# Kernel tuning notes

Hardware: AMD Instinct MI355X
Metric: run time of the kernel (lower is better)

The kernel has to match this reference:

```python
import jax, jax.numpy as jnp
import numpy as np

TAU = 0.02        # System2Reasoner softmax temperature
TOP_K = 50        # retrieval top-k
ALPHA = 1.0       # visual/text prototype mixing
TAU_CONF = 0.8    # entropy confidence threshold


def _normalize(x):
    return x / jnp.maximum(jnp.linalg.norm(x, axis=-1, keepdims=True), 1e-12)


def _entropy(logits):
    p = jax.nn.softmax(logits, axis=-1)
    return -jnp.sum(p * jnp.log(p + 1e-10))


def setup_inputs() -> dict:
    key = jax.random.key(0)
    k1, k2, k3, k4, k5, k6 = jax.random.split(key, 6)
    D, P, M, C = 768, 2048, 65536, 1000
    test_global = _normalize(jax.random.normal(k1, (1, D), dtype=jnp.float32))
    test_patches = _normalize(jax.random.normal(k2, (P, D), dtype=jnp.float32))
    memory_nodes = _normalize(jax.random.normal(k3, (M, D), dtype=jnp.float32))
    textual_anchors = _normalize(jax.random.normal(k4, (C, D), dtype=jnp.float32))
    class_sums = jax.random.normal(k5, (C, D), dtype=jnp.float32)
    class_counts = jax.random.uniform(k6, (C,), dtype=jnp.float32) * 100.0 + 1.0
    return {
        "test_global": test_global,
        "test_patches": test_patches,
        "memory_nodes": memory_nodes,
        "textual_anchors": textual_anchors,
        "class_sums": class_sums,
        "class_counts": class_counts,
        "max_steps": 3,
    }


def reference(test_global, test_patches, memory_nodes, textual_anchors,
              class_sums, class_counts, max_steps):
    # System-1 prototypes
    safe_counts = jnp.maximum(class_counts, 1.0)[:, None]            # [C,1]
    visual_protos = _normalize(class_sums / safe_counts)             # [C,D]
    protos = _normalize(textual_anchors + ALPHA * visual_protos)     # [C,D]

    sys1_logits = 100.0 * test_global @ protos.T                     # [1,C]
    active0 = _entropy(sys1_logits) > TAU_CONF

    def body(carry, _):
        patches, logits, step, active = carry
        # message passing: topk cosine-sim retrieval + softmax-weighted gather
        sim = patches @ memory_nodes.T                               # [P,M]
        topv, topi = jax.lax.top_k(sim, TOP_K)                       # [P,K]
        attn = jax.nn.softmax(topv / TAU, axis=1)                    # [P,K]
        gathered = memory_nodes[topi]                                # [P,K,D]
        messages = jnp.einsum('pk,pkd->pd', attn, gathered)          # [P,D]
        new_patches = _normalize(patches + messages)
        # token evidence pooling
        ev = jnp.max(new_patches @ textual_anchors.T, axis=-1, keepdims=True)  # [P,1]
        w = jax.nn.softmax(ev / TAU, axis=0)                         # [P,1]
        g = _normalize(jnp.sum(new_patches * w, axis=0, keepdims=True))        # [1,D]
        new_logits = 100.0 * g @ protos.T                            # [1,C]
        # only commit updates while the entropy loop is still active
        patches = jnp.where(active, new_patches, patches)
        logits = jnp.where(active, new_logits, logits)
        step = step + active.astype(jnp.int32)
        active = jnp.logical_and(active, _entropy(new_logits) > TAU_CONF)
        return (patches, logits, step, active), None

    (patches, final_logits, step, _), _ = jax.lax.scan(
        body, (test_patches, sys1_logits, jnp.int32(0), active0),
        None, length=max_steps)
    return final_logits, step
```

## Files before the change

### kernel.cpp

```cpp
#include <hip/hip_runtime.h>
#include <hip/hip_bf16.h>
#include <stdint.h>


typedef __attribute__((ext_vector_type(8))) short short8;
typedef __attribute__((ext_vector_type(4))) float f32x4;

#define DIM    768
#define NPATCH 2048
#define NMEM   65536
#define NCLS   1000
#define NSAMP  4096
#define CAP    1024
#define PRESEL 64
#define PCAP   128
#define TAUINV 50.0f

__device__ __forceinline__ unsigned short f2bf(float f){
  unsigned b = __float_as_uint(f);
  b += 0x7FFFu + ((b >> 16) & 1u);
  return (unsigned short)(b >> 16);
}
__device__ __forceinline__ unsigned encf(float x){
  unsigned b = __float_as_uint(x);
  return (b & 0x80000000u) ? ~b : (b | 0x80000000u);
}
__device__ __forceinline__ float decf(unsigned k){
  unsigned b = (k & 0x80000000u) ? (k & 0x7FFFFFFFu) : ~k;
  return __uint_as_float(b);
}
__device__ __forceinline__ void gload16(const void* g, void* l){
  __builtin_amdgcn_global_load_lds(
      (const __attribute__((address_space(1))) unsigned int*)g,
      (__attribute__((address_space(3))) unsigned int*)l, 16, 0, 0);
}
__device__ __forceinline__ uint4 pack8(float4 a, float4 b){
  uint4 u;
  u.x = (unsigned)f2bf(a.x) | ((unsigned)f2bf(a.y) << 16);
  u.y = (unsigned)f2bf(a.z) | ((unsigned)f2bf(a.w) << 16);
  u.z = (unsigned)f2bf(b.x) | ((unsigned)f2bf(b.y) << 16);
  u.w = (unsigned)f2bf(b.z) | ((unsigned)f2bf(b.w) << 16);
  return u;
}

__device__ __forceinline__ unsigned select_kth(const unsigned* keys, int n, int k,
                                               unsigned* hist, int t)
{
  __syncthreads();
  if (t == 0){ hist[256] = 0u; hist[257] = (unsigned)k; }
  __syncthreads();
  for (int pass = 0; pass < 4; ++pass){
    int shift = 24 - 8*pass;
    hist[t] = 0u;
    __syncthreads();
    unsigned pref = hist[256];
    for (int i = t; i < n; i += 256){
      unsigned key = keys[i];
      bool ok = (pass == 0) || ((key >> (shift + 8)) == pref);
      if (ok) atomicAdd(&hist[(key >> shift) & 255u], 1u);
    }
    __syncthreads();
    if (t == 0){
      unsigned krem = hist[257];
      unsigned cum = 0u; int b = 255;
      for (; b >= 0; --b){ cum += hist[b]; if (cum >= krem) break; }
      if (b < 0) b = 0;
      unsigned above = cum - hist[b];
      hist[257] = krem - above;
      hist[256] = (pref << 8) | (unsigned)b;
    }
    __syncthreads();
  }
  return hist[256];
}

__global__ __launch_bounds__(256) void proto_kernel(
    const float* __restrict__ anchors, const float* __restrict__ sums,
    const float* __restrict__ counts, float* __restrict__ protos,
    unsigned short* __restrict__ anchors_bf)
{
  int c = blockIdx.x, t = threadIdx.x;
  if (c >= NCLS){
    for (int j = 0; j < 3; ++j) anchors_bf[(size_t)c*DIM + t + j*256] = 0;
    return;
  }
  __shared__ float wv[4]; __shared__ float bc;
  float cnt = fmaxf(counts[c], 1.0f);
  float v[3];
  #pragma unroll
  for (int j = 0; j < 3; ++j) v[j] = sums[(size_t)c*DIM + t + j*256] / cnt;
  float ss = v[0]*v[0] + v[1]*v[1] + v[2]*v[2];
  for (int off = 32; off > 0; off >>= 1) ss += __shfl_down(ss, off, 64);
  if ((t & 63) == 0) wv[t >> 6] = ss;
  __syncthreads();
  if (t == 0) bc = wv[0] + wv[1] + wv[2] + wv[3];
  __syncthreads();
  float rn = 1.0f / fmaxf(sqrtf(bc), 1e-12f);
  __syncthreads();
  float pr[3];
  #pragma unroll
  for (int j = 0; j < 3; ++j){
    int d = t + j*256;
    float a = anchors[(size_t)c*DIM + d];
    pr[j] = a + v[j] * rn;
    int dd = (d & ~63) | ((((d >> 3) ^ c) & 7) << 3) | (d & 7);
    anchors_bf[(size_t)c*DIM + dd] = f2bf(a);
  }
  ss = pr[0]*pr[0] + pr[1]*pr[1] + pr[2]*pr[2];
  for (int off = 32; off > 0; off >>= 1) ss += __shfl_down(ss, off, 64);
  if ((t & 63) == 0) wv[t >> 6] = ss;
  __syncthreads();
  if (t == 0) bc = wv[0] + wv[1] + wv[2] + wv[3];
  __syncthreads();
  float rn2 = 1.0f / fmaxf(sqrtf(bc), 1e-12f);
  #pragma unroll
  for (int j = 0; j < 3; ++j) protos[(size_t)c*DIM + t + j*256] = pr[j] * rn2;
}

__global__ __launch_bounds__(256) void prep_patches(
    const float* __restrict__ tp, float* __restrict__ pc)
{
  size_t i = (size_t)blockIdx.x*256 + threadIdx.x;
  *(float4*)(pc + i*4) = *(const float4*)(tp + i*4);
}

__global__ __launch_bounds__(256) void conv_kernel(
    const float* __restrict__ src, unsigned short* __restrict__ dst)
{
  int id = blockIdx.x*256 + threadIdx.x;
  int row = id / 12, blk = id % 12;
  const float4* s = (const float4*)(src + (size_t)row*DIM + blk*64);
  unsigned short* drow = dst + (size_t)row*DIM + blk*64;
  int key = row & 7;
  #pragma unroll
  for (int c8 = 0; c8 < 8; ++c8){
    uint4 u = pack8(s[c8*2], s[c8*2+1]);
    *(uint4*)(drow + (c8 ^ key)*8) = u;
  }
}

__global__ __launch_bounds__(192) void slab_kernel(
    const float* __restrict__ pc, unsigned short* __restrict__ slab)
{
  int b = blockIdx.x, t = threadIdx.x;
  int p = b*2 + (t >= 96 ? 1 : 0);
  int q = (t >= 96) ? t - 96 : t;
  int ks = q >> 3, c8 = q & 7;
  const float* s = pc + (size_t)p*DIM + ks*64 + c8*8;
  uint4 u = pack8(*(const float4*)s, *(const float4*)(s + 4));
  *(uint4*)((char*)slab + (((size_t)ks*NPATCH + p)*128) + ((size_t)(c8 ^ (p & 7))*16)) = u;
}

template<int MODE, int NT>
__global__ __launch_bounds__(256, 3) void gemm_kernel(
    const unsigned short* __restrict__ Abf, int rowbase,
    const unsigned short* __restrict__ Bslab,
    const float* __restrict__ thresholds,
    int* __restrict__ counters,
    int* __restrict__ cand_idx,
    float* __restrict__ cand_score,
    float* __restrict__ sims_sample,
    unsigned* __restrict__ ev_key,
    const int* __restrict__ active)
{
  if (*active == 0) return;
  __shared__ __align__(16) unsigned short Al[128*64];
  __shared__ __align__(16) unsigned short Bl[128*64];
  int b = blockIdx.x, nwg = gridDim.x;
  int wg = (b & 7)*(nwg >> 3) + (b >> 3);
  int mt0 = (wg >> 4) * NT, pt = wg & 15;
  int t = threadIdx.x, w = t >> 6, lane = t & 63, l15 = lane & 15, l4 = lane >> 4;
  int wr = w >> 1, wc = w & 1;
  int pbase = pt*128;
  int srow = w*8 + (lane >> 3);
  int scol = (lane & 7)*16;

  const char* Ab = (const char*)Abf;
  const char* Bb = (const char*)Bslab;

  float thv[4];
  if (MODE == 0){
    #pragma unroll
    for (int g = 0; g < 4; ++g) thv[g] = thresholds[pbase + wc*64 + g*16 + l15];
  }

  f32x4 acc[4][4];
  #pragma unroll
  for (int x = 0; x < 4; ++x)
    #pragma unroll
    for (int y = 0; y < 4; ++y) acc[x][y] = (f32x4){0.f, 0.f, 0.f, 0.f};

  const int NSTEP = NT * 12;
  for (int s = 0; s < NSTEP; ++s){
    int tile = s / 12, ks = s % 12;
    if (s) __syncthreads();
    size_t arow0 = (size_t)rowbase + ((size_t)(mt0 + tile))*128;
    #pragma unroll
    for (int i = 0; i < 4; ++i){
      const void* ga = Ab + ((arow0 + srow + i*32)*(size_t)(DIM*2)) + ks*128 + scol;
      gload16(ga, (char*)Al + i*4096 + w*1024);
      const void* gb = Bb + (((size_t)ks*NPATCH + pbase)*128) + i*4096 + w*1024 + lane*16;
      gload16(gb, (char*)Bl + i*4096 + w*1024);
    }
    __syncthreads();

    short8 af[2][4], bf_[2][4];
    #pragma unroll
    for (int kk = 0; kk < 2; ++kk){
      #pragma unroll
      for (int ng = 0; ng < 4; ++ng){
        int row = wr*64 + ng*16 + l15;
        int slot = (kk*4 + l4) ^ (row & 7);
        af[kk][ng] = *(const short8*)((const char*)Al + row*128 + slot*16);
      }
      #pragma unroll
      for (int g = 0; g < 4; ++g){
        int row = wc*64 + g*16 + l15;
        int slot = (kk*4 + l4) ^ (row & 7);
        bf_[kk][g] = *(const short8*)((const char*)Bl + row*128 + slot*16);
      }
    }
    #pragma unroll
    for (int kk = 0; kk < 2; ++kk)
      #pragma unroll
      for (int ng = 0; ng < 4; ++ng)
        #pragma unroll
        for (int g = 0; g < 4; ++g)
          acc[ng][g] = __builtin_amdgcn_mfma_f32_16x16x32_bf16(af[kk][ng], bf_[kk][g], acc[ng][g], 0, 0, 0);

    if (ks == 11){
      int nodebase = rowbase + (mt0 + tile)*128 + wr*64;
      if (MODE == 0){
        #pragma unroll
        for (int g = 0; g < 4; ++g){
          int patch = pbase + wc*64 + g*16 + l15;
          float th = thv[g];
          #pragma unroll
          for (int ng = 0; ng < 4; ++ng){
            #pragma unroll
            for (int i = 0; i < 4; ++i){
              float v = acc[ng][g][i];
              if (v >= th){
                int node = nodebase + ng*16 + l4*4 + i;
                int pos = atomicAdd(&counters[patch], 1);
                if (pos < CAP){
                  cand_idx[(size_t)patch*CAP + pos]   = node;
                  cand_score[(size_t)patch*CAP + pos] = v;
                }
              }
            }
          }
        }
      } else if (MODE == 1){
        #pragma unroll
        for (int g = 0; g < 4; ++g){
          int patch = pbase + wc*64 + g*16 + l15;
          #pragma unroll
          for (int ng = 0; ng < 4; ++ng){
            int col = nodebase + ng*16 + l4*4;
            *(f32x4*)(sims_sample + (size_t)patch*NSAMP + col) = acc[ng][g];
          }
        }
      } else {
        #pragma unroll
        for (int g = 0; g < 4; ++g){
          int patch = pbase + wc*64 + g*16 + l15;
          float m = -3e38f; bool any = false;
          #pragma unroll
          for (int ng = 0; ng < 4; ++ng){
            #pragma unroll
            for (int i = 0; i < 4; ++i){
              int a = nodebase + ng*16 + l4*4 + i;
              if (a < NCLS){ m = fmaxf(m, acc[ng][g][i]); any = true; }
            }
          }
          if (any) atomicMax(&ev_key[patch], encf(m));
        }
      }
      if (tile + 1 < NT){
        #pragma unroll
        for (int x = 0; x < 4; ++x)
          #pragma unroll
          for (int y = 0; y < 4; ++y) acc[x][y] = (f32x4){0.f, 0.f, 0.f, 0.f};
      }
    }
  }
}

__global__ __launch_bounds__(256) void thresh_kernel(
    const float* __restrict__ sims, float* __restrict__ thresholds,
    int* __restrict__ counters, int* __restrict__ cand_idx,
    float* __restrict__ cand_score, unsigned* __restrict__ ev_key,
    const int* __restrict__ active)
{
  if (*active == 0) return;
  __shared__ unsigned keys[NSAMP];
  __shared__ unsigned hist[258];
  __shared__ int lcnt;
  int p = blockIdx.x, t = threadIdx.x;
  const float4* src = (const float4*)(sims + (size_t)p*NSAMP);
  for (int i = t; i < NSAMP/4; i += 256){
    float4 v = src[i];
    keys[i*4+0] = encf(v.x); keys[i*4+1] = encf(v.y);
    keys[i*4+2] = encf(v.z); keys[i*4+3] = encf(v.w);
  }
  unsigned kth = select_kth(keys, NSAMP, 16, hist, t);
  if (t == 0){ thresholds[p] = decf(kth); ev_key[p] = 0u; lcnt = 0; }
  __syncthreads();
  for (int i = t; i < NSAMP; i += 256){
    unsigned key = keys[i];
    if (key >= kth){
      int pos = atomicAdd(&lcnt, 1);
      if (pos < CAP){
        cand_idx[(size_t)p*CAP + pos]   = i;
        cand_score[(size_t)p*CAP + pos] = decf(key);
      }
    }
  }
  __syncthreads();
  if (t == 0) counters[p] = lcnt < CAP ? lcnt : CAP;
}

__global__ __launch_bounds__(256) void msg_kernel(
    const int* __restrict__ counters, const int* __restrict__ cand_idx,
    const float* __restrict__ cand_score, const float* __restrict__ memf,
    float* __restrict__ pc, unsigned short* __restrict__ slab,
    const int* __restrict__ active)
{
  if (*active == 0) return;
  __shared__ unsigned sk[CAP]; __shared__ int si[CAP];
  __shared__ __align__(16) float gl[DIM];
  __shared__ unsigned hist[258];
  __shared__ int pn[PCAP]; __shared__ float pv[PCAP];
  __shared__ float selv[64]; __shared__ int seli[64]; __shared__ float attn[64];
  __shared__ float wv[4]; __shared__ float bc;
  __shared__ int cnt2;
  int p = blockIdx.x, t = threadIdx.x;
  int n = counters[p]; if (n > CAP) n = CAP;
  #pragma unroll
  for (int j = 0; j < 3; ++j) gl[t + j*256] = pc[(size_t)p*DIM + t + j*256];
  for (int i = t; i < CAP; i += 256){
    sk[i] = (i < n) ? encf(cand_score[(size_t)p*CAP + i]) : 0u;
    si[i] = (i < n) ? cand_idx[(size_t)p*CAP + i] : 0;
  }
  unsigned kth64 = 1u;
  if (n > PRESEL) kth64 = select_kth(sk, n, PRESEL, hist, t);
  else            __syncthreads();
  if (t == 0) cnt2 = 0;
  __syncthreads();
  for (int i = t; i < n; i += 256){
    if (sk[i] >= kth64){
      int pos = atomicAdd(&cnt2, 1);
      if (pos < PCAP) pn[pos] = si[i];
    }
  }
  __syncthreads();
  int m = cnt2 < PCAP ? cnt2 : PCAP;
  int w = t >> 6, lane = t & 63;
  for (int i = w; i < m; i += 4){
    const float* row = memf + (size_t)pn[i]*DIM;
    float s = 0.f;
    #pragma unroll
    for (int j = 0; j < 12; ++j){
      int d = lane + j*64;
      s += row[d] * gl[d];
    }
    for (int off = 32; off > 0; off >>= 1) s += __shfl_down(s, off, 64);
    if (lane == 0) pv[i] = s;
  }
  __syncthreads();
  int K = m < 50 ? m : 50;
  if (t < m) sk[t] = encf(pv[t]);
  unsigned kth50 = 1u;
  if (m > K) kth50 = select_kth(sk, m, K, hist, t);
  else       __syncthreads();
  if (t == 0) cnt2 = 0;
  __syncthreads();
  if (t < m && sk[t] > kth50){
    int pos = atomicAdd(&cnt2, 1);
    seli[pos] = pn[t]; selv[pos] = pv[t];
    sk[t] = 0u;
  }
  __syncthreads();
  if (t == 0){
    int c = cnt2;
    for (int j = c; j < K; ++j){
      int best = -1, bestnode = 0x7FFFFFFF;
      for (int i = 0; i < m; ++i)
        if (sk[i] == kth50 && pn[i] < bestnode){ best = i; bestnode = pn[i]; }
      if (best < 0) break;
      seli[j] = pn[best]; selv[j] = pv[best]; sk[best] = 0u;
    }
  }
  __syncthreads();
  float v = (t < K) ? selv[t] : -3e38f;
  for (int off = 32; off > 0; off >>= 1) v = fmaxf(v, __shfl_down(v, off, 64));
  if ((t & 63) == 0) wv[t >> 6] = v;
  __syncthreads();
  if (t == 0) bc = fmaxf(fmaxf(wv[0], wv[1]), fmaxf(wv[2], wv[3]));
  __syncthreads();
  float vmax = bc;
  __syncthreads();
  if (t < K) attn[t] = __expf((selv[t] - vmax) * TAUINV);
  __syncthreads();
  if (t == 0){ float s = 0.f; for (int k = 0; k < K; ++k) s += attn[k]; bc = s; }
  __syncthreads();
  float inv = 1.0f / bc;
  int d0 = t, d1 = t + 256, d2 = t + 512;
  float a0 = gl[d0], a1 = gl[d1], a2 = gl[d2];
  for (int k = 0; k < K; ++k){
    float a = attn[k] * inv;
    const float* row = memf + (size_t)seli[k]*DIM;
    a0 += a * row[d0]; a1 += a * row[d1]; a2 += a * row[d2];
  }
  float ss = a0*a0 + a1*a1 + a2*a2;
  for (int off = 32; off > 0; off >>= 1) ss += __shfl_down(ss, off, 64);
  if ((t & 63) == 0) wv[t >> 6] = ss;
  __syncthreads();
  if (t == 0) bc = wv[0] + wv[1] + wv[2] + wv[3];
  __syncthreads();
  float rn = 1.0f / fmaxf(sqrtf(bc), 1e-12f);
  a0 *= rn; a1 *= rn; a2 *= rn;
  float* orow = pc + (size_t)p*DIM;
  orow[d0] = a0; orow[d1] = a1; orow[d2] = a2;
  __syncthreads();
  gl[d0] = a0; gl[d1] = a1; gl[d2] = a2;
  __syncthreads();
  if (t < 96){
    int ks2 = t >> 3, c8 = t & 7;
    const float* sblk = &gl[ks2*64 + c8*8];
    uint4 u = pack8(*(const float4*)sblk, *(const float4*)(sblk + 4));
    *(uint4*)((char*)slab + (((size_t)ks2*NPATCH + p)*128) + ((size_t)(c8 ^ (p & 7))*16)) = u;
  }
}

__global__ __launch_bounds__(256) void pl2_kernel(
    const unsigned* __restrict__ ev_key, const float* __restrict__ pc,
    float* __restrict__ g_part, const int* __restrict__ active)
{
  if (*active == 0) return;
  __shared__ float wv[4]; __shared__ float bc;
  int t = threadIdx.x;
  float m = -3e38f;
  for (int i = t; i < NPATCH; i += 256) m = fmaxf(m, decf(ev_key[i]));
  for (int off = 32; off > 0; off >>= 1) m = fmaxf(m, __shfl_down(m, off, 64));
  if ((t & 63) == 0) wv[t >> 6] = m;
  __syncthreads();
  if (t == 0) bc = fmaxf(fmaxf(wv[0], wv[1]), fmaxf(wv[2], wv[3]));
  __syncthreads();
  float M = bc;
  __syncthreads();
  float s = 0.f;
  for (int i = t; i < NPATCH; i += 256) s += __expf((decf(ev_key[i]) - M) * TAUINV);
  for (int off = 32; off > 0; off >>= 1) s += __shfl_down(s, off, 64);
  if ((t & 63) == 0) wv[t >> 6] = s;
  __syncthreads();
  if (t == 0) bc = wv[0] + wv[1] + wv[2] + wv[3];
  __syncthreads();
  float invS = 1.0f / bc;
  int pbase = blockIdx.x * 64;
  float a0 = 0.f, a1 = 0.f, a2 = 0.f;
  for (int i = 0; i < 64; ++i){
    int p = pbase + i;
    float wgt = __expf((decf(ev_key[p]) - M) * TAUINV) * invS;
    const float* row = pc + (size_t)p*DIM;
    a0 += wgt * row[t]; a1 += wgt * row[t + 256]; a2 += wgt * row[t + 512];
  }
  g_part[blockIdx.x*DIM + t]       = a0;
  g_part[blockIdx.x*DIM + t + 256] = a1;
  g_part[blockIdx.x*DIM + t + 512] = a2;
}

template<bool INIT>
__global__ __launch_bounds__(256) void cm_kernel(
    const float* __restrict__ gsrc, const float* __restrict__ protos,
    float* __restrict__ logits_cur, int* __restrict__ step, int* __restrict__ active)
{
  if (!INIT && *active == 0) return;
  __shared__ __align__(16) float gl[DIM];
  __shared__ float lg[NCLS];
  __shared__ float wv[4]; __shared__ float bc;
  int t = threadIdx.x;
  if (INIT){
    #pragma unroll
    for (int j = 0; j < 3; ++j) gl[t + j*256] = gsrc[t + j*256];
  } else {
    float gv[3]; float ss = 0.f;
    #pragma unroll
    for (int j = 0; j < 3; ++j){
      int d = t + j*256;
      float s = 0.f;
      for (int b2 = 0; b2 < 32; ++b2) s += gsrc[b2*DIM + d];
      gv[j] = s; ss += s*s;
    }
    for (int off = 32; off > 0; off >>= 1) ss += __shfl_down(ss, off, 64);
    if ((t & 63) == 0) wv[t >> 6] = ss;
    __syncthreads();
    if (t == 0) bc = wv[0] + wv[1] + wv[2] + wv[3];
    __syncthreads();
    float rn = 1.0f / fmaxf(sqrtf(bc), 1e-12f);
    #pragma unroll
    for (int j = 0; j < 3; ++j) gl[t + j*256] = gv[j] * rn;
  }
  __syncthreads();
  for (int c = t; c < NCLS; c += 256){
    const float4* pr = (const float4*)(protos + (size_t)c*DIM);
    float s = 0.f;
    #pragma unroll 4
    for (int d4 = 0; d4 < DIM/4; ++d4){
      float4 pv = pr[d4];
      float4 gv = *(const float4*)&gl[d4*4];
      s += gv.x*pv.x + gv.y*pv.y + gv.z*pv.z + gv.w*pv.w;
    }
    float L = 100.0f * s;
    lg[c] = L; logits_cur[c] = L;
  }
  __syncthreads();
  float m = -3e38f;
  for (int c = t; c < NCLS; c += 256) m = fmaxf(m, lg[c]);
  for (int off = 32; off > 0; off >>= 1) m = fmaxf(m, __shfl_down(m, off, 64));
  if ((t & 63) == 0) wv[t >> 6] = m;
  __syncthreads();
  if (t == 0) bc = fmaxf(fmaxf(wv[0], wv[1]), fmaxf(wv[2], wv[3]));
  __syncthreads();
  float M = bc;
  __syncthreads();
  float s = 0.f;
  for (int c = t; c < NCLS; c += 256) s += __expf(lg[c] - M);
  for (int off = 32; off > 0; off >>= 1) s += __shfl_down(s, off, 64);
  if ((t & 63) == 0) wv[t >> 6] = s;
  __syncthreads();
  if (t == 0) bc = wv[0] + wv[1] + wv[2] + wv[3];
  __syncthreads();
  float S = bc;
  __syncthreads();
  float hp = 0.f;
  for (int c = t; c < NCLS; c += 256){
    float pcl = __expf(lg[c] - M) / S;
    hp += pcl * __logf(pcl + 1e-10f);
  }
  for (int off = 32; off > 0; off >>= 1) hp += __shfl_down(hp, off, 64);
  if ((t & 63) == 0) wv[t >> 6] = hp;
  __syncthreads();
  if (t == 0){
    float H = -(wv[0] + wv[1] + wv[2] + wv[3]);
    if (INIT){ *step = 0; *active = (H > 0.8f) ? 1 : 0; }
    else     { *step = *step + 1; *active = (H > 0.8f) ? 1 : 0; }
  }
}

__global__ void pub_kernel(const float* __restrict__ logits_cur, const int* __restrict__ step,
                           float* __restrict__ out)
{
  int i = blockIdx.x*256 + threadIdx.x;
  if (i < NCLS) out[i] = logits_cur[i];
  else if (i == NCLS) out[i] = (float)(*step);
}

extern "C" void kernel_launch(void* const* d_in, const int* in_sizes, int n_in,
                              void* d_out, int out_size, void* d_ws, size_t ws_size,
                              hipStream_t stream)
{
  (void)in_sizes; (void)n_in; (void)out_size; (void)ws_size;
  const float* tg  = (const float*)d_in[0];
  const float* tp  = (const float*)d_in[1];
  const float* mem = (const float*)d_in[2];
  const float* anc = (const float*)d_in[3];
  const float* cs  = (const float*)d_in[4];
  const float* cc  = (const float*)d_in[5];

  char* ws = (char*)d_ws;
  auto al = [](size_t x){ return (x + 255) & ~(size_t)255; };
  size_t OFF_PC   = 0;
  size_t OFF_PROT = al(OFF_PC   + (size_t)NPATCH*DIM*4);
  size_t OFF_ABF  = al(OFF_PROT + (size_t)NCLS*DIM*4);
  size_t OFF_MBF  = al(OFF_ABF  + (size_t)1024*DIM*2);
  size_t OFF_SLAB = al(OFF_MBF  + (size_t)NMEM*DIM*2);
  size_t OFF_SS   = al(OFF_SLAB + (size_t)NPATCH*DIM*2);
  size_t OFF_THR  = al(OFF_SS   + (size_t)NPATCH*NSAMP*4);
  size_t OFF_CNT  = al(OFF_THR  + (size_t)NPATCH*4);
  size_t OFF_CI   = al(OFF_CNT  + (size_t)NPATCH*4);
  size_t OFF_CSC  = al(OFF_CI   + (size_t)NPATCH*CAP*4);
  size_t OFF_EV   = al(OFF_CSC  + (size_t)NPATCH*CAP*4);
  size_t OFF_GP   = al(OFF_EV   + (size_t)NPATCH*4);
  size_t OFF_LC   = al(OFF_GP   + (size_t)32*DIM*4);
  size_t OFF_STEP = al(OFF_LC   + (size_t)NCLS*4);

  float*          pc      = (float*)(ws + OFF_PC);
  float*          protos  = (float*)(ws + OFF_PROT);
  unsigned short* abf     = (unsigned short*)(ws + OFF_ABF);
  unsigned short* mbf     = (unsigned short*)(ws + OFF_MBF);
  unsigned short* slab    = (unsigned short*)(ws + OFF_SLAB);
  float*          simss   = (float*)(ws + OFF_SS);
  float*          thr     = (float*)(ws + OFF_THR);
  int*            cnt     = (int*)(ws + OFF_CNT);
  int*            ci      = (int*)(ws + OFF_CI);
  float*          csc     = (float*)(ws + OFF_CSC);
  unsigned*       evk     = (unsigned*)(ws + OFF_EV);
  float*          gp      = (float*)(ws + OFF_GP);
  float*          lc      = (float*)(ws + OFF_LC);
  int*            stepp   = (int*)(ws + OFF_STEP);
  int*            activep = stepp + 1;

  proto_kernel<<<1024, 256, 0, stream>>>(anc, cs, cc, protos, abf);
  prep_patches<<<(NPATCH*DIM/4)/256, 256, 0, stream>>>(tp, pc);
  conv_kernel<<<(NMEM*12)/256, 256, 0, stream>>>(mem, mbf);
  cm_kernel<true><<<1, 256, 0, stream>>>(tg, protos, lc, stepp, activep);
  slab_kernel<<<NPATCH/2, 192, 0, stream>>>(pc, slab);

  for (int it = 0; it < 3; ++it){
    gemm_kernel<1,1><<<(NSAMP/128)*16, 256, 0, stream>>>(mbf, 0, slab, thr, cnt, ci, csc, simss, evk, activep);
    thresh_kernel<<<NPATCH, 256, 0, stream>>>(simss, thr, cnt, ci, csc, evk, activep);
    gemm_kernel<0,4><<<((NMEM-NSAMP)/512)*16, 256, 0, stream>>>(mbf, NSAMP, slab, thr, cnt, ci, csc, simss, evk, activep);
    msg_kernel<<<NPATCH, 256, 0, stream>>>(cnt, ci, csc, mem, pc, slab, activep);
    gemm_kernel<2,1><<<(1024/128)*16, 256, 0, stream>>>(abf, 0, slab, thr, cnt, ci, csc, simss, evk, activep);
    pl2_kernel<<<32, 256, 0, stream>>>(evk, pc, gp, activep);
    cm_kernel<false><<<1, 256, 0, stream>>>(gp, protos, lc, stepp, activep);
  }
  pub_kernel<<<4, 256, 0, stream>>>(lc, stepp, (float*)d_out);
}
```

Measured before the change: 2.010 ms.

## Quantize memory nodes and patches to int8 for retrieval similarity GEMMs

Memory nodes and patches are now quantized to int8 with per-row scales, and the sampling and candidate-threshold GEMMs use i8 MFMA (16x16x64) instead of bf16. Scores are rescaled in the epilogue before thresholding and candidate collection. The evidence GEMM against text anchors stays in bf16 as a separate kernel. This halves the operand bytes and doubles MFMA throughput per instruction. The cost is coarser similarity estimates, which may shift thresholds and candidate sets, although the final messages are still computed from fp32 scores.

```diff
diff --git a/kernel.cpp b/kernel.cpp
--- a/kernel.cpp
+++ b/kernel.cpp
@@ -5,6 +5,7 @@
 
 typedef __attribute__((ext_vector_type(8))) short short8;
 typedef __attribute__((ext_vector_type(4))) float f32x4;
+typedef __attribute__((ext_vector_type(4))) int   i32x4;
 
 #define DIM    768
 #define NPATCH 2048
@@ -42,6 +43,21 @@
   u.w = (unsigned)f2bf(b.z) | ((unsigned)f2bf(b.w) << 16);
   return u;
 }
+__device__ __forceinline__ uint4 packq16(const float* s, float inv){
+  unsigned wd[4];
+  #pragma unroll
+  for (int k = 0; k < 4; ++k){
+    unsigned v = 0;
+    #pragma unroll
+    for (int j = 0; j < 4; ++j){
+      int q = __float2int_rn(s[k*4 + j] * inv);
+      q = q > 127 ? 127 : (q < -127 ? -127 : q);
+      v |= ((unsigned)(q & 255)) << (8*j);
+    }
+    wd[k] = v;
+  }
+  return make_uint4(wd[0], wd[1], wd[2], wd[3]);
+}
 
 __device__ __forceinline__ unsigned select_kth(const unsigned* keys, int n, int k,
                                                unsigned* hist, int t)
@@ -124,71 +140,98 @@
   *(float4*)(pc + i*4) = *(const float4*)(tp + i*4);
 }
 
-__global__ __launch_bounds__(256) void conv_kernel(
-    const float* __restrict__ src, unsigned short* __restrict__ dst)
-{
-  int id = blockIdx.x*256 + threadIdx.x;
-  int row = id / 12, blk = id % 12;
-  const float4* s = (const float4*)(src + (size_t)row*DIM + blk*64);
-  unsigned short* drow = dst + (size_t)row*DIM + blk*64;
-  int key = row & 7;
-  #pragma unroll
-  for (int c8 = 0; c8 < 8; ++c8){
-    uint4 u = pack8(s[c8*2], s[c8*2+1]);
-    *(uint4*)(drow + (c8 ^ key)*8) = u;
-  }
-}
-
-__global__ __launch_bounds__(192) void slab_kernel(
-    const float* __restrict__ pc, unsigned short* __restrict__ slab)
-{
-  int b = blockIdx.x, t = threadIdx.x;
-  int p = b*2 + (t >= 96 ? 1 : 0);
-  int q = (t >= 96) ? t - 96 : t;
-  int ks = q >> 3, c8 = q & 7;
-  const float* s = pc + (size_t)p*DIM + ks*64 + c8*8;
-  uint4 u = pack8(*(const float4*)s, *(const float4*)(s + 4));
-  *(uint4*)((char*)slab + (((size_t)ks*NPATCH + p)*128) + ((size_t)(c8 ^ (p & 7))*16)) = u;
+__global__ __launch_bounds__(512) void conv_i8_kernel(
+    const float* __restrict__ src, signed char* __restrict__ dst,
+    float* __restrict__ scales)
+{
+  int w = threadIdx.x >> 6, lane = threadIdx.x & 63;
+  int row = blockIdx.x*8 + w;
+  const float* r = src + (size_t)row*DIM;
+  float x[16]; float mx = 0.f;
+  if (lane < 48){
+    #pragma unroll
+    for (int j = 0; j < 4; ++j){
+      float4 v = *(const float4*)(r + lane*16 + j*4);
+      x[j*4+0] = v.x; x[j*4+1] = v.y; x[j*4+2] = v.z; x[j*4+3] = v.w;
+      mx = fmaxf(mx, fmaxf(fmaxf(fabsf(v.x), fabsf(v.y)), fmaxf(fabsf(v.z), fabsf(v.w))));
+    }
+  }
+  for (int off = 32; off > 0; off >>= 1) mx = fmaxf(mx, __shfl_xor(mx, off, 64));
+  if (lane == 0) scales[row] = mx / 127.0f;
+  float inv = (mx > 0.f) ? 127.0f / mx : 0.f;
+  if (lane < 48){
+    int ks = lane >> 2, c = lane & 3;
+    uint4 u = packq16(x, inv);
+    *(uint4*)(dst + (size_t)row*DIM + ks*64 + ((c ^ (row & 3))*16)) = u;
+  }
+}
+
+__global__ __launch_bounds__(256) void slab_init(
+    const float* __restrict__ pc, unsigned short* __restrict__ slab,
+    signed char* __restrict__ sli8, float* __restrict__ spb)
+{
+  __shared__ __align__(16) float gl[DIM];
+  __shared__ float wv[4]; __shared__ float bc;
+  int p = blockIdx.x, t = threadIdx.x;
+  float a0 = pc[(size_t)p*DIM + t], a1 = pc[(size_t)p*DIM + t + 256],
+        a2 = pc[(size_t)p*DIM + t + 512];
+  gl[t] = a0; gl[t + 256] = a1; gl[t + 512] = a2;
+  float am = fmaxf(fabsf(a0), fmaxf(fabsf(a1), fabsf(a2)));
+  for (int off = 32; off > 0; off >>= 1) am = fmaxf(am, __shfl_down(am, off, 64));
+  if ((t & 63) == 0) wv[t >> 6] = am;
+  __syncthreads();
+  if (t == 0) bc = fmaxf(fmaxf(wv[0], wv[1]), fmaxf(wv[2], wv[3]));
+  __syncthreads();
+  float mx = bc;
+  float inv8 = (mx > 0.f) ? 127.0f / mx : 0.f;
+  if (t < 96){
+    int ks2 = t >> 3, c8 = t & 7;
+    const float* sblk = &gl[ks2*64 + c8*8];
+    uint4 u = pack8(*(const float4*)sblk, *(const float4*)(sblk + 4));
+    *(uint4*)((char*)slab + (((size_t)ks2*NPATCH + p)*128) + ((size_t)(c8 ^ (p & 7))*16)) = u;
+  }
+  if (t < 48){
+    int ks2 = t >> 2, c = t & 3;
+    uint4 u = packq16(&gl[t*16], inv8);
+    *(uint4*)(sli8 + ((size_t)ks2*NPATCH + p)*64 + ((c ^ (p & 3))*16)) = u;
+  }
+  if (t == 0) spb[p] = mx / 127.0f;
 }
 
 template<int MODE, int NT>
-__global__ __launch_bounds__(256, 3) void gemm_kernel(
-    const unsigned short* __restrict__ Abf, int rowbase,
-    const unsigned short* __restrict__ Bslab,
+__global__ __launch_bounds__(256, 3) void gemm8_kernel(
+    const signed char* __restrict__ Ai8, const float* __restrict__ sA, int rowbase,
+    const signed char* __restrict__ Bslab, const float* __restrict__ sB,
     const float* __restrict__ thresholds,
     int* __restrict__ counters,
     int* __restrict__ cand_idx,
     float* __restrict__ cand_score,
     float* __restrict__ sims_sample,
-    unsigned* __restrict__ ev_key,
     const int* __restrict__ active)
 {
   if (*active == 0) return;
-  __shared__ __align__(16) unsigned short Al[128*64];
-  __shared__ __align__(16) unsigned short Bl[128*64];
+  __shared__ __align__(16) signed char Al[128*64];
+  __shared__ __align__(16) signed char Bl[128*64];
   int b = blockIdx.x, nwg = gridDim.x;
   int wg = (b & 7)*(nwg >> 3) + (b >> 3);
   int mt0 = (wg >> 4) * NT, pt = wg & 15;
   int t = threadIdx.x, w = t >> 6, lane = t & 63, l15 = lane & 15, l4 = lane >> 4;
   int wr = w >> 1, wc = w & 1;
   int pbase = pt*128;
-  int srow = w*8 + (lane >> 3);
-  int scol = (lane & 7)*16;
-
-  const char* Ab = (const char*)Abf;
-  const char* Bb = (const char*)Bslab;
-
-  float thv[4];
-  if (MODE == 0){
-    #pragma unroll
-    for (int g = 0; g < 4; ++g) thv[g] = thresholds[pbase + wc*64 + g*16 + l15];
-  }
-
-  f32x4 acc[4][4];
+
+  float thv[4], sbv[4];
+  #pragma unroll
+  for (int g = 0; g < 4; ++g){
+    int patch = pbase + wc*64 + g*16 + l15;
+    if (MODE == 0) thv[g] = thresholds[patch];
+    sbv[g] = sB[patch];
+  }
+
+  i32x4 acc[4][4];
   #pragma unroll
   for (int x = 0; x < 4; ++x)
     #pragma unroll
-    for (int y = 0; y < 4; ++y) acc[x][y] = (f32x4){0.f, 0.f, 0.f, 0.f};
+    for (int y = 0; y < 4; ++y) acc[x][y] = (i32x4){0, 0, 0, 0};
 
   const int NSTEP = NT * 12;
   for (int s = 0; s < NSTEP; ++s){
@@ -196,14 +239,119 @@
     if (s) __syncthreads();
     size_t arow0 = (size_t)rowbase + ((size_t)(mt0 + tile))*128;
     #pragma unroll
+    for (int i = 0; i < 2; ++i){
+      int g = w*64 + i*256 + lane;
+      const void* ga = Ai8 + (arow0 + (g >> 2))*(size_t)DIM + ks*64 + (g & 3)*16;
+      gload16(ga, (char*)Al + (w*64 + i*256)*16);
+      const void* gb = Bslab + ((size_t)ks*NPATCH + pbase)*64 + (size_t)g*16;
+      gload16(gb, (char*)Bl + (w*64 + i*256)*16);
+    }
+    __syncthreads();
+
+    i32x4 af[4], bfr[4];
+    #pragma unroll
+    for (int ng = 0; ng < 4; ++ng){
+      int row = wr*64 + ng*16 + l15;
+      af[ng] = *(const i32x4*)(Al + row*64 + ((l4 ^ (row & 3))*16));
+    }
+    #pragma unroll
+    for (int g = 0; g < 4; ++g){
+      int row = wc*64 + g*16 + l15;
+      bfr[g] = *(const i32x4*)(Bl + row*64 + ((l4 ^ (row & 3))*16));
+    }
+    #pragma unroll
+    for (int ng = 0; ng < 4; ++ng)
+      #pragma unroll
+      for (int g = 0; g < 4; ++g)
+        acc[ng][g] = __builtin_amdgcn_mfma_i32_16x16x64_i8(af[ng], bfr[g], acc[ng][g], 0, 0, 0);
+
+    if (ks == 11){
+      int nodebase = rowbase + (mt0 + tile)*128 + wr*64;
+      if (MODE == 0){
+        #pragma unroll
+        for (int g = 0; g < 4; ++g){
+          int patch = pbase + wc*64 + g*16 + l15;
+          float th = thv[g], sb = sbv[g];
+          #pragma unroll
+          for (int ng = 0; ng < 4; ++ng){
+            f32x4 sa = *(const f32x4*)(sA + nodebase + ng*16 + l4*4);
+            #pragma unroll
+            for (int i = 0; i < 4; ++i){
+              float v = (float)acc[ng][g][i] * sa[i] * sb;
+              if (v >= th){
+                int node = nodebase + ng*16 + l4*4 + i;
+                int pos = atomicAdd(&counters[patch], 1);
+                if (pos < CAP){
+                  cand_idx[(size_t)patch*CAP + pos]   = node;
+                  cand_score[(size_t)patch*CAP + pos] = v;
+                }
+              }
+            }
+          }
+        }
+      } else {
+        #pragma unroll
+        for (int g = 0; g < 4; ++g){
+          int patch = pbase + wc*64 + g*16 + l15;
+          float sb = sbv[g];
+          #pragma unroll
+          for (int ng = 0; ng < 4; ++ng){
+            f32x4 sa = *(const f32x4*)(sA + nodebase + ng*16 + l4*4);
+            f32x4 v;
+            #pragma unroll
+            for (int i = 0; i < 4; ++i) v[i] = (float)acc[ng][g][i] * sa[i] * sb;
+            int col = nodebase + ng*16 + l4*4;
+            *(f32x4*)(sims_sample + (size_t)patch*NSAMP + col) = v;
+          }
+        }
+      }
+      if (tile + 1 < NT){
+        #pragma unroll
+        for (int x = 0; x < 4; ++x)
+          #pragma unroll
+          for (int y = 0; y < 4; ++y) acc[x][y] = (i32x4){0, 0, 0, 0};
+      }
+    }
+  }
+}
+
+__global__ __launch_bounds__(256, 3) void gemm_ev_kernel(
+    const unsigned short* __restrict__ Abf,
+    const unsigned short* __restrict__ Bslab,
+    unsigned* __restrict__ ev_key,
+    const int* __restrict__ active)
+{
+  if (*active == 0) return;
+  __shared__ __align__(16) unsigned short Al[128*64];
+  __shared__ __align__(16) unsigned short Bl[128*64];
+  int b = blockIdx.x, nwg = gridDim.x;
+  int wg = (b & 7)*(nwg >> 3) + (b >> 3);
+  int mt = wg >> 4, pt = wg & 15;
+  int t = threadIdx.x, w = t >> 6, lane = t & 63, l15 = lane & 15, l4 = lane >> 4;
+  int wr = w >> 1, wc = w & 1;
+  int pbase = pt*128;
+  int srow = w*8 + (lane >> 3);
+  int scol = (lane & 7)*16;
+  const char* Ab = (const char*)Abf;
+  const char* Bb = (const char*)Bslab;
+
+  f32x4 acc[4][4];
+  #pragma unroll
+  for (int x = 0; x < 4; ++x)
+    #pragma unroll
+    for (int y = 0; y < 4; ++y) acc[x][y] = (f32x4){0.f, 0.f, 0.f, 0.f};
+
+  for (int s = 0; s < 12; ++s){
+    if (s) __syncthreads();
+    size_t arow0 = (size_t)mt*128;
+    #pragma unroll
     for (int i = 0; i < 4; ++i){
-      const void* ga = Ab + ((arow0 + srow + i*32)*(size_t)(DIM*2)) + ks*128 + scol;
+      const void* ga = Ab + ((arow0 + srow + i*32)*(size_t)(DIM*2)) + s*128 + scol;
       gload16(ga, (char*)Al + i*4096 + w*1024);
-      const void* gb = Bb + (((size_t)ks*NPATCH + pbase)*128) + i*4096 + w*1024 + lane*16;
+      const void* gb = Bb + (((size_t)s*NPATCH + pbase)*128) + i*4096 + w*1024 + lane*16;
       gload16(gb, (char*)Bl + i*4096 + w*1024);
     }
     __syncthreads();
-
     short8 af[2][4], bf_[2][4];
     #pragma unroll
     for (int kk = 0; kk < 2; ++kk){
@@ -227,63 +375,21 @@
         #pragma unroll
         for (int g = 0; g < 4; ++g)
           acc[ng][g] = __builtin_amdgcn_mfma_f32_16x16x32_bf16(af[kk][ng], bf_[kk][g], acc[ng][g], 0, 0, 0);
-
-    if (ks == 11){
-      int nodebase = rowbase + (mt0 + tile)*128 + wr*64;
-      if (MODE == 0){
-        #pragma unroll
-        for (int g = 0; g < 4; ++g){
-          int patch = pbase + wc*64 + g*16 + l15;
-          float th = thv[g];
-          #pragma unroll
-          for (int ng = 0; ng < 4; ++ng){
-            #pragma unroll
-            for (int i = 0; i < 4; ++i){
-              float v = acc[ng][g][i];
-              if (v >= th){
-                int node = nodebase + ng*16 + l4*4 + i;
-                int pos = atomicAdd(&counters[patch], 1);
-                if (pos < CAP){
-                  cand_idx[(size_t)patch*CAP + pos]   = node;
-                  cand_score[(size_t)patch*CAP + pos] = v;
-                }
-              }
-            }
-          }
-        }
-      } else if (MODE == 1){
-        #pragma unroll
-        for (int g = 0; g < 4; ++g){
-          int patch = pbase + wc*64 + g*16 + l15;
-          #pragma unroll
-          for (int ng = 0; ng < 4; ++ng){
-            int col = nodebase + ng*16 + l4*4;
-            *(f32x4*)(sims_sample + (size_t)patch*NSAMP + col) = acc[ng][g];
-          }
-        }
-      } else {
-        #pragma unroll
-        for (int g = 0; g < 4; ++g){
-          int patch = pbase + wc*64 + g*16 + l15;
-          float m = -3e38f; bool any = false;
-          #pragma unroll
-          for (int ng = 0; ng < 4; ++ng){
-            #pragma unroll
-            for (int i = 0; i < 4; ++i){
-              int a = nodebase + ng*16 + l4*4 + i;
-              if (a < NCLS){ m = fmaxf(m, acc[ng][g][i]); any = true; }
-            }
-          }
-          if (any) atomicMax(&ev_key[patch], encf(m));
-        }
+  }
+
+  #pragma unroll
+  for (int g = 0; g < 4; ++g){
+    int patch = pbase + wc*64 + g*16 + l15;
+    float m = -3e38f; bool any = false;
+    #pragma unroll
+    for (int ng = 0; ng < 4; ++ng){
+      #pragma unroll
+      for (int i = 0; i < 4; ++i){
+        int a = mt*128 + wr*64 + ng*16 + l4*4 + i;
+        if (a < NCLS){ m = fmaxf(m, acc[ng][g][i]); any = true; }
       }
-      if (tile + 1 < NT){
-        #pragma unroll
-        for (int x = 0; x < 4; ++x)
-          #pragma unroll
-          for (int y = 0; y < 4; ++y) acc[x][y] = (f32x4){0.f, 0.f, 0.f, 0.f};
-      }
-    }
+    }
+    if (any) atomicMax(&ev_key[patch], encf(m));
   }
 }
 
@@ -325,6 +431,7 @@
     const int* __restrict__ counters, const int* __restrict__ cand_idx,
     const float* __restrict__ cand_score, const float* __restrict__ memf,
     float* __restrict__ pc, unsigned short* __restrict__ slab,
+    signed char* __restrict__ sli8, float* __restrict__ spb,
     const int* __restrict__ active)
 {
   if (*active == 0) return;
@@ -423,15 +530,28 @@
   a0 *= rn; a1 *= rn; a2 *= rn;
   float* orow = pc + (size_t)p*DIM;
   orow[d0] = a0; orow[d1] = a1; orow[d2] = a2;
+  float am = fmaxf(fabsf(a0), fmaxf(fabsf(a1), fabsf(a2)));
+  for (int off = 32; off > 0; off >>= 1) am = fmaxf(am, __shfl_down(am, off, 64));
   __syncthreads();
   gl[d0] = a0; gl[d1] = a1; gl[d2] = a2;
-  __syncthreads();
+  if ((t & 63) == 0) wv[t >> 6] = am;
+  __syncthreads();
+  if (t == 0) bc = fmaxf(fmaxf(wv[0], wv[1]), fmaxf(wv[2], wv[3]));
+  __syncthreads();
+  float mx = bc;
+  float inv8 = (mx > 0.f) ? 127.0f / mx : 0.f;
   if (t < 96){
     int ks2 = t >> 3, c8 = t & 7;
     const float* sblk = &gl[ks2*64 + c8*8];
     uint4 u = pack8(*(const float4*)sblk, *(const float4*)(sblk + 4));
     *(uint4*)((char*)slab + (((size_t)ks2*NPATCH + p)*128) + ((size_t)(c8 ^ (p & 7))*16)) = u;
   }
+  if (t < 48){
+    int ks2 = t >> 2, c = t & 3;
+    uint4 u = packq16(&gl[t*16], inv8);
+    *(uint4*)(sli8 + ((size_t)ks2*NPATCH + p)*64 + ((c ^ (p & 3))*16)) = u;
+  }
+  if (t == 0) spb[p] = mx / 127.0f;
 }
 
 __global__ __launch_bounds__(256) void pl2_kernel(
@@ -574,9 +694,12 @@
   size_t OFF_PC   = 0;
   size_t OFF_PROT = al(OFF_PC   + (size_t)NPATCH*DIM*4);
   size_t OFF_ABF  = al(OFF_PROT + (size_t)NCLS*DIM*4);
-  size_t OFF_MBF  = al(OFF_ABF  + (size_t)1024*DIM*2);
-  size_t OFF_SLAB = al(OFF_MBF  + (size_t)NMEM*DIM*2);
-  size_t OFF_SS   = al(OFF_SLAB + (size_t)NPATCH*DIM*2);
+  size_t OFF_MI8  = al(OFF_ABF  + (size_t)1024*DIM*2);
+  size_t OFF_SA   = al(OFF_MI8  + (size_t)NMEM*DIM);
+  size_t OFF_SLAB = al(OFF_SA   + (size_t)NMEM*4);
+  size_t OFF_SLI8 = al(OFF_SLAB + (size_t)NPATCH*DIM*2);
+  size_t OFF_SPB  = al(OFF_SLI8 + (size_t)NPATCH*DIM);
+  size_t OFF_SS   = al(OFF_SPB  + (size_t)NPATCH*4);
   size_t OFF_THR  = al(OFF_SS   + (size_t)NPATCH*NSAMP*4);
   size_t OFF_CNT  = al(OFF_THR  + (size_t)NPATCH*4);
   size_t OFF_CI   = al(OFF_CNT  + (size_t)NPATCH*4);
@@ -589,8 +712,11 @@
   float*          pc      = (float*)(ws + OFF_PC);
   float*          protos  = (float*)(ws + OFF_PROT);
   unsigned short* abf     = (unsigned short*)(ws + OFF_ABF);
-  unsigned short* mbf     = (unsigned short*)(ws + OFF_MBF);
+  signed char*    mi8     = (signed char*)(ws + OFF_MI8);
+  float*          sa      = (float*)(ws + OFF_SA);
   unsigned short* slab    = (unsigned short*)(ws + OFF_SLAB);
+  signed char*    sli8    = (signed char*)(ws + OFF_SLI8);
+  float*          spb     = (float*)(ws + OFF_SPB);
   float*          simss   = (float*)(ws + OFF_SS);
   float*          thr     = (float*)(ws + OFF_THR);
   int*            cnt     = (int*)(ws + OFF_CNT);
@@ -604,16 +730,18 @@
 
   proto_kernel<<<1024, 256, 0, stream>>>(anc, cs, cc, protos, abf);
   prep_patches<<<(NPATCH*DIM/4)/256, 256, 0, stream>>>(tp, pc);
-  conv_kernel<<<(NMEM*12)/256, 256, 0, stream>>>(mem, mbf);
+  conv_i8_kernel<<<NMEM/8, 512, 0, stream>>>(mem, mi8, sa);
   cm_kernel<true><<<1, 256, 0, stream>>>(tg, protos, lc, stepp, activep);
-  slab_kernel<<<NPATCH/2, 192, 0, stream>>>(pc, slab);
+  slab_init<<<NPATCH, 256, 0, stream>>>(pc, slab, sli8, spb);
 
   for (int it = 0; it < 3; ++it){
-    gemm_kernel<1,1><<<(NSAMP/128)*16, 256, 0, stream>>>(mbf, 0, slab, thr, cnt, ci, csc, simss, evk, activep);
+    gemm8_kernel<1,1><<<(NSAMP/128)*16, 256, 0, stream>>>(
+        mi8, sa, 0, sli8, spb, thr, cnt, ci, csc, simss, activep);
     thresh_kernel<<<NPATCH, 256, 0, stream>>>(simss, thr, cnt, ci, csc, evk, activep);
-    gemm_kernel<0,4><<<((NMEM-NSAMP)/512)*16, 256, 0, stream>>>(mbf, NSAMP, slab, thr, cnt, ci, csc, simss, evk, activep);
-    msg_kernel<<<NPATCH, 256, 0, stream>>>(cnt, ci, csc, mem, pc, slab, activep);
-    gemm_kernel<2,1><<<(1024/128)*16, 256, 0, stream>>>(abf, 0, slab, thr, cnt, ci, csc, simss, evk, activep);
+    gemm8_kernel<0,4><<<((NMEM-NSAMP)/512)*16, 256, 0, stream>>>(
+        mi8, sa, NSAMP, sli8, spb, thr, cnt, ci, csc, simss, activep);
+    msg_kernel<<<NPATCH, 256, 0, stream>>>(cnt, ci, csc, mem, pc, slab, sli8, spb, activep);
+    gemm_ev_kernel<<<(1024/128)*16, 256, 0, stream>>>(abf, slab, evk, activep);
     pl2_kernel<<<32, 256, 0, stream>>>(evk, pc, gp, activep);
     cm_kernel<false><<<1, 256, 0, stream>>>(gp, protos, lc, stepp, activep);
   }
```

After: 1.760 ms. 1.14x faster.
